# Kernel tuning notes

Measured on AMD Instinct MI355X. Metric: run time of the kernel, lower is better.

## Reference

```python
import jax, jax.numpy as jnp
import numpy as np

DIM = 1024
NUM_HEADS = 16
DPH = DIM // NUM_HEADS
B, S = 4, 2048
LN_EPS = 1e-5


def layer_norm(x, g, b):
    mu = jnp.mean(x, axis=-1, keepdims=True)
    var = jnp.mean((x - mu) ** 2, axis=-1, keepdims=True)
    return (x - mu) * jax.lax.rsqrt(var + LN_EPS) * g + b


def setup_inputs() -> dict:
    key = jax.random.key(0)
    ks = jax.random.split(key, 10)
    sd = 0.02
    return {
        "x": jax.random.normal(ks[0], (B, S, DIM), dtype=jnp.float32),
        "Wq": jax.random.normal(ks[1], (DIM, DIM), dtype=jnp.float32) * sd,
        "Wk": jax.random.normal(ks[2], (DIM, DIM), dtype=jnp.float32) * sd,
        "Wv": jax.random.normal(ks[3], (DIM, DIM), dtype=jnp.float32) * sd,
        "bq": jnp.zeros((DIM,), dtype=jnp.float32),
        "bk": jnp.zeros((DIM,), dtype=jnp.float32),
        "bv": jnp.zeros((DIM,), dtype=jnp.float32),
        "ln1_g": jnp.ones((DIM,), dtype=jnp.float32),
        "ln1_b": jnp.zeros((DIM,), dtype=jnp.float32),
        "W1": jax.random.normal(ks[4], (DIM, 4 * DIM), dtype=jnp.float32) * sd,
        "b1": jnp.zeros((4 * DIM,), dtype=jnp.float32),
        "W2": jax.random.normal(ks[5], (4 * DIM, DIM), dtype=jnp.float32) * sd,
        "b2": jnp.zeros((DIM,), dtype=jnp.float32),
        "ln2_g": jnp.ones((DIM,), dtype=jnp.float32),
        "ln2_b": jnp.zeros((DIM,), dtype=jnp.float32),
    }


def reference(x, Wq, Wk, Wv, bq, bk, bv, ln1_g, ln1_b, W1, b1, W2, b2, ln2_g, ln2_b):
    b, s, d = x.shape
    # QKV projections (heads are independent linears -> one fused GEMM each)
    q = (x @ Wq + bq).reshape(b, s, NUM_HEADS, DPH)
    k = (x @ Wk + bk).reshape(b, s, NUM_HEADS, DPH)
    v = (x @ Wv + bv).reshape(b, s, NUM_HEADS, DPH)
    # Faithful quirk: module scales by 1/sqrt(dph) twice => 1/dph total
    scores = jnp.einsum("bqhd,bkhd->bhqk", q, k) / DPH
    causal = jnp.tril(jnp.ones((s, s), dtype=bool))
    scores = jnp.where(causal, scores, -1e9)
    attn = jax.nn.softmax(scores, axis=-1)
    out_attn = jnp.einsum("bhqk,bkhd->bqhd", attn, v).reshape(b, s, d)
    # Add & Norm 1 (no output projection in original)
    h = layer_norm(out_attn + x, ln1_g, ln1_b)
    # Feed-forward (dropout is identity at eval)
    ffn = jax.nn.relu(h @ W1 + b1) @ W2 + b2
    # Add & Norm 2
    return layer_norm(ffn + h, ln2_g, ln2_b)
```

## Files before the change

### kernel.cpp

```cpp
#include <hip/hip_runtime.h>
#include <hip/hip_bf16.h>

typedef __bf16 bf16_t;
typedef __bf16 bf16x8 __attribute__((ext_vector_type(8)));
typedef __bf16 bf16x4 __attribute__((ext_vector_type(4)));
typedef float  floatx4 __attribute__((ext_vector_type(4)));

#define DIM    1024
#define S_LEN  2048
#define NHEAD  16

template <typename T>
__device__ __forceinline__ bf16x8 load8bf(const T* src) {
  if constexpr (sizeof(T) == 2) {
    return *reinterpret_cast<const bf16x8*>(src);
  } else {
    floatx4 f0 = *reinterpret_cast<const floatx4*>(src);
    floatx4 f1 = *reinterpret_cast<const floatx4*>(src + 4);
    bf16x8 h;
    h[0] = (bf16_t)f0[0]; h[1] = (bf16_t)f0[1];
    h[2] = (bf16_t)f0[2]; h[3] = (bf16_t)f0[3];
    h[4] = (bf16_t)f1[0]; h[5] = (bf16_t)f1[1];
    h[6] = (bf16_t)f1[2]; h[7] = (bf16_t)f1[3];
    return h;
  }
}

__global__ __launch_bounds__(256) void convT3(
    const float* __restrict__ in0, int ldi0, bf16_t* __restrict__ out0,
    const float* __restrict__ in1, int ldi1, bf16_t* __restrict__ out1,
    const float* __restrict__ in2, int ldi2, bf16_t* __restrict__ out2,
    int ldo) {
  __shared__ bf16_t tile[32][33];
  const int z = blockIdx.z;
  const float* in = (z == 0) ? in0 : ((z == 1) ? in1 : in2);
  bf16_t* out = (z == 0) ? out0 : ((z == 1) ? out1 : out2);
  int ldi = (z == 0) ? ldi0 : ((z == 1) ? ldi1 : ldi2);
  int tx = threadIdx.x, ty = threadIdx.y;
  int n0 = blockIdx.x * 32, k0 = blockIdx.y * 32;
#pragma unroll
  for (int i = 0; i < 4; ++i)
    tile[ty + 8 * i][tx] = (bf16_t)in[(size_t)(k0 + ty + 8 * i) * ldi + n0 + tx];
  __syncthreads();
#pragma unroll
  for (int i = 0; i < 4; ++i)
    out[(size_t)(n0 + ty + 8 * i) * ldo + k0 + tx] = tile[tx][ty + 8 * i];
}

#define BM 128
#define BN 128
#define BK 32
#define LSTR 40

template <typename TA>
__global__ __launch_bounds__(256) void gemm_abt(
    const TA* __restrict__ A, int lda,
    const bf16_t* __restrict__ Bt, int zBRow,
    bf16_t* __restrict__ C, int ldc, int zCOff,
    const float* __restrict__ bias0, const float* __restrict__ bias1,
    const float* __restrict__ bias2,
    int K, int relu, int accum) {
  __shared__ bf16_t As[BM * LSTR];
  __shared__ bf16_t Bs[BN * LSTR];
  const int z = blockIdx.z;
  const float* bias = (z == 0) ? bias0 : ((z == 1) ? bias1 : bias2);
  const bf16_t* Bz = Bt + (size_t)z * zBRow * K;
  C += (size_t)z * zCOff;

  const int tid  = threadIdx.x;
  const int lane = tid & 63;
  const int wave = tid >> 6;
  const int wr   = wave >> 1;
  const int wc   = wave & 1;
  const int quad = lane >> 4;
  const int l15  = lane & 15;
  const int m0   = blockIdx.y * BM;
  const int n0   = blockIdx.x * BN;

  floatx4 acc[4][4];
#pragma unroll
  for (int i = 0; i < 4; ++i)
#pragma unroll
    for (int j = 0; j < 4; ++j) acc[i][j] = (floatx4)(0.0f);

  const int kIters = K / BK;
  for (int kt = 0; kt < kIters; ++kt) {
#pragma unroll
    for (int p = 0; p < 2; ++p) {
      int id  = p * 256 + tid;
      int row = id >> 2;
      int c8  = (id & 3) * 8;
      *reinterpret_cast<bf16x8*>(&As[row * LSTR + c8]) =
          load8bf(A + (size_t)(m0 + row) * lda + kt * BK + c8);
      *reinterpret_cast<bf16x8*>(&Bs[row * LSTR + c8]) =
          *reinterpret_cast<const bf16x8*>(Bz + (size_t)(n0 + row) * K + kt * BK + c8);
    }
    __syncthreads();

    bf16x8 a[4], b[4];
#pragma unroll
    for (int i = 0; i < 4; ++i)
      a[i] = *reinterpret_cast<const bf16x8*>(&As[(wr * 64 + i * 16 + l15) * LSTR + quad * 8]);
#pragma unroll
    for (int j = 0; j < 4; ++j)
      b[j] = *reinterpret_cast<const bf16x8*>(&Bs[(wc * 64 + j * 16 + l15) * LSTR + quad * 8]);
#pragma unroll
    for (int i = 0; i < 4; ++i)
#pragma unroll
      for (int j = 0; j < 4; ++j)
        acc[i][j] = __builtin_amdgcn_mfma_f32_16x16x32_bf16(a[i], b[j], acc[i][j], 0, 0, 0);
    __syncthreads();
  }

#pragma unroll
  for (int j = 0; j < 4; ++j) {
    int gn = n0 + wc * 64 + j * 16 + l15;
    float bv = bias ? bias[gn] : 0.0f;
#pragma unroll
    for (int i = 0; i < 4; ++i) {
      int gm = m0 + wr * 64 + i * 16 + quad * 4;
#pragma unroll
      for (int r = 0; r < 4; ++r) {
        float v = acc[i][j][r] + bv;
        if (relu) v = fmaxf(v, 0.0f);
        size_t idx = (size_t)(gm + r) * ldc + gn;
        if (accum) v += (float)C[idx];
        C[idx] = (bf16_t)v;
      }
    }
  }
}

__global__ __launch_bounds__(256) void transpose_v(const bf16_t* __restrict__ in,
                                                   bf16_t* __restrict__ outp) {
  __shared__ bf16_t tile[32][33];
  int tx = threadIdx.x, ty = threadIdx.y;
  int s0 = blockIdx.x * 32, d0 = blockIdx.y * 32, bh = blockIdx.z;
  int z = bh >> 4, h = bh & 15;
  const bf16_t* src = in + (size_t)z * S_LEN * 3072 + 2048 + h * 64;
#pragma unroll
  for (int i = 0; i < 4; ++i)
    tile[ty + 8 * i][tx] = src[(size_t)(s0 + ty + 8 * i) * 3072 + d0 + tx];
  __syncthreads();
  bf16_t* dst = outp + (size_t)bh * 64 * S_LEN;
#pragma unroll
  for (int i = 0; i < 4; ++i)
    dst[(size_t)(d0 + ty + 8 * i) * S_LEN + s0 + tx] = tile[tx][ty + 8 * i];
}

#define TQ  64
#define TK  64
#define AST 72
#define QSCALE 0.02254211f

struct KVregs { bf16x8 k[2]; bf16x8 v[2]; };

__global__ __launch_bounds__(256, 2) void attn_mfma2(
    const bf16_t* __restrict__ qkv, const bf16_t* __restrict__ vt,
    float* __restrict__ out) {
  __shared__ bf16_t QsPs[TQ * AST];
  __shared__ bf16_t Ks[TK * AST];
  __shared__ bf16_t Vs[TK * AST];

  const int tid  = threadIdx.x;
  const int lane = tid & 63;
  const int w    = tid >> 6;
  const int quad = lane >> 4;
  const int l15  = lane & 15;
  const int pi   = blockIdx.x;
  const int h    = blockIdx.y;
  const int z    = blockIdx.z;
  const int qb2[2] = {pi, 31 - pi};
  const bf16_t* qkv_b = qkv + (size_t)z * S_LEN * 3072;
  const bf16_t* vt_bh = vt + ((size_t)z * NHEAD + h) * 64 * S_LEN;
  float* out_b = out + (size_t)z * S_LEN * DIM;

  const int ktEnd = qb2[1] + 1;

  auto kv_load = [&](KVregs& r, int kt) {
#pragma unroll
    for (int p = 0; p < 2; ++p) {
      int id  = p * 256 + tid;
      int row = id >> 3;
      int c8  = (id & 7) * 8;
      r.k[p] = *reinterpret_cast<const bf16x8*>(
          qkv_b + (size_t)(kt * TK + row) * 3072 + 1024 + h * 64 + c8);
      r.v[p] = *reinterpret_cast<const bf16x8*>(
          vt_bh + (size_t)row * S_LEN + kt * TK + c8);
    }
  };
  auto kv_write = [&](KVregs& r) {
#pragma unroll
    for (int p = 0; p < 2; ++p) {
      int id  = p * 256 + tid;
      int row = id >> 3;
      int c8  = (id & 7) * 8;
      *reinterpret_cast<bf16x8*>(&Ks[row * AST + c8]) = r.k[p];
      *reinterpret_cast<bf16x8*>(&Vs[row * AST + c8]) = r.v[p];
    }
  };

  KVregs RA, RB;
  kv_load(RA, 0);

  bf16x8 aq[2][2];
  for (int tile = 0; tile < 2; ++tile) {
    if (tile) __syncthreads();
    const int qg0 = qb2[tile] * TQ;
#pragma unroll
    for (int p = 0; p < 2; ++p) {
      int id  = p * 256 + tid;
      int row = id >> 3;
      int c8  = (id & 7) * 8;
      bf16x8 v = *reinterpret_cast<const bf16x8*>(
          qkv_b + (size_t)(qg0 + row) * 3072 + h * 64 + c8);
      bf16x8 o;
#pragma unroll
      for (int e = 0; e < 8; ++e) o[e] = (bf16_t)((float)v[e] * QSCALE);
      *reinterpret_cast<bf16x8*>(&QsPs[row * AST + c8]) = o;
    }
    __syncthreads();
#pragma unroll
    for (int ks = 0; ks < 2; ++ks)
      aq[tile][ks] = *reinterpret_cast<const bf16x8*>(
          &QsPs[(w * 16 + l15) * AST + ks * 32 + quad * 8]);
  }

  float lp[2][4];
  floatx4 O[2][4];
#pragma unroll
  for (int t = 0; t < 2; ++t)
#pragma unroll
    for (int r = 0; r < 4; ++r) lp[t][r] = 0.0f;
#pragma unroll
  for (int t = 0; t < 2; ++t)
#pragma unroll
    for (int dt = 0; dt < 4; ++dt) O[t][dt] = (floatx4)(0.0f);

  auto step = [&](int kt, KVregs& cur, KVregs& nxt) {
    if (kt + 1 < ktEnd) kv_load(nxt, kt + 1);
    asm volatile("s_waitcnt lgkmcnt(0)" ::: "memory");
    __builtin_amdgcn_s_barrier();
    kv_write(cur);
    asm volatile("s_waitcnt lgkmcnt(0)" ::: "memory");
    __builtin_amdgcn_s_barrier();

    bf16x8 bk[4][2], bv[4][2];
#pragma unroll
    for (int i = 0; i < 4; ++i)
#pragma unroll
      for (int ks = 0; ks < 2; ++ks) {
        bk[i][ks] = *reinterpret_cast<const bf16x8*>(
            &Ks[(i * 16 + l15) * AST + ks * 32 + quad * 8]);
        bv[i][ks] = *reinterpret_cast<const bf16x8*>(
            &Vs[(i * 16 + l15) * AST + ks * 32 + quad * 8]);
      }

#pragma unroll
    for (int tile = 0; tile < 2; ++tile) {
      const int qtb = qb2[tile] * TQ + w * 16;
      if (kt * TK > qtb + 15) continue;

      floatx4 s[4];
      __builtin_amdgcn_s_setprio(1);
#pragma unroll
      for (int ktl = 0; ktl < 4; ++ktl) {
        s[ktl] = __builtin_amdgcn_mfma_f32_16x16x32_bf16(
            aq[tile][0], bk[ktl][0], (floatx4)(0.0f), 0, 0, 0);
        s[ktl] = __builtin_amdgcn_mfma_f32_16x16x32_bf16(
            aq[tile][1], bk[ktl][1], s[ktl], 0, 0, 0);
      }
      __builtin_amdgcn_s_setprio(0);
      if (kt * TK + TK - 1 > qtb) {
#pragma unroll
        for (int ktl = 0; ktl < 4; ++ktl) {
          int gk = kt * TK + ktl * 16 + l15;
#pragma unroll
          for (int r = 0; r < 4; ++r) {
            int gq = qtb + quad * 4 + r;
            if (gk > gq) s[ktl][r] = -1e30f;
          }
        }
      }
#pragma unroll
      for (int ktl = 0; ktl < 4; ++ktl)
#pragma unroll
        for (int r = 0; r < 4; ++r) {
          float p = exp2f(s[ktl][r]);
          lp[tile][r] += p;
          QsPs[(w * 16 + quad * 4 + r) * AST + ktl * 16 + l15] = (bf16_t)p;
        }

      bf16x8 ap0 = *reinterpret_cast<const bf16x8*>(
          &QsPs[(w * 16 + l15) * AST + quad * 8]);
      bf16x8 ap1 = *reinterpret_cast<const bf16x8*>(
          &QsPs[(w * 16 + l15) * AST + 32 + quad * 8]);
      __builtin_amdgcn_s_setprio(1);
#pragma unroll
      for (int dt = 0; dt < 4; ++dt) {
        O[tile][dt] = __builtin_amdgcn_mfma_f32_16x16x32_bf16(
            ap0, bv[dt][0], O[tile][dt], 0, 0, 0);
        O[tile][dt] = __builtin_amdgcn_mfma_f32_16x16x32_bf16(
            ap1, bv[dt][1], O[tile][dt], 0, 0, 0);
      }
      __builtin_amdgcn_s_setprio(0);
    }
  };

  for (int kt = 0; kt < ktEnd; kt += 2) {
    step(kt, RA, RB);
    if (kt + 1 < ktEnd) step(kt + 1, RB, RA);
  }

#pragma unroll
  for (int tile = 0; tile < 2; ++tile) {
    const int qg0 = qb2[tile] * TQ;
    float inv[4];
#pragma unroll
    for (int r = 0; r < 4; ++r) {
      float lv = lp[tile][r];
#pragma unroll
      for (int off = 1; off < 16; off <<= 1) lv += __shfl_xor(lv, off);
      inv[r] = 1.0f / lv;
    }
#pragma unroll
    for (int dt = 0; dt < 4; ++dt)
#pragma unroll
      for (int r = 0; r < 4; ++r)
        out_b[(size_t)(qg0 + w * 16 + quad * 4 + r) * DIM +
              h * 64 + dt * 16 + l15] = O[tile][dt][r] * inv[r];
  }
}

template <typename TA>
__global__ __launch_bounds__(256) void add_ln_k(const TA* a,
                                                const float* b,
                                                const float* __restrict__ g,
                                                const float* __restrict__ be,
                                                float* out) {
  const int row = blockIdx.x;
  const int t   = threadIdx.x;
  const size_t base = (size_t)row * DIM;

  float x[4];
  {
    floatx4 bv = *reinterpret_cast<const floatx4*>(b + base + t * 4);
    if constexpr (sizeof(TA) == 2) {
      bf16x4 av = *reinterpret_cast<const bf16x4*>(a + base + t * 4);
#pragma unroll
      for (int i = 0; i < 4; ++i) x[i] = (float)av[i] + bv[i];
    } else {
      floatx4 av = *reinterpret_cast<const floatx4*>(a + base + t * 4);
#pragma unroll
      for (int i = 0; i < 4; ++i) x[i] = av[i] + bv[i];
    }
  }
  float s1 = 0.0f, s2 = 0.0f;
#pragma unroll
  for (int i = 0; i < 4; ++i) { s1 += x[i]; s2 += x[i] * x[i]; }
#pragma unroll
  for (int off = 32; off; off >>= 1) {
    s1 += __shfl_xor(s1, off);
    s2 += __shfl_xor(s2, off);
  }
  __shared__ float ls1[4], ls2[4];
  if ((t & 63) == 0) { ls1[t >> 6] = s1; ls2[t >> 6] = s2; }
  __syncthreads();
  float S1 = ls1[0] + ls1[1] + ls1[2] + ls1[3];
  float S2 = ls2[0] + ls2[1] + ls2[2] + ls2[3];
  float mu  = S1 * (1.0f / DIM);
  float var = S2 * (1.0f / DIM) - mu * mu;
  float rs  = rsqrtf(var + 1e-5f);
#pragma unroll
  for (int i = 0; i < 4; ++i) {
    int c = t * 4 + i;
    out[base + c] = (x[i] - mu) * rs * g[c] + be[c];
  }
}

extern "C" void kernel_launch(void* const* d_in, const int* in_sizes, int n_in,
                              void* d_out, int out_size, void* d_ws, size_t ws_size,
                              hipStream_t stream) {
  const float* x   = (const float*)d_in[0];
  const float* Wq  = (const float*)d_in[1];
  const float* Wk  = (const float*)d_in[2];
  const float* Wv  = (const float*)d_in[3];
  const float* bq  = (const float*)d_in[4];
  const float* bk  = (const float*)d_in[5];
  const float* bv  = (const float*)d_in[6];
  const float* g1  = (const float*)d_in[7];
  const float* be1 = (const float*)d_in[8];
  const float* W1  = (const float*)d_in[9];
  const float* b1  = (const float*)d_in[10];
  const float* W2  = (const float*)d_in[11];
  const float* b2  = (const float*)d_in[12];
  const float* g2  = (const float*)d_in[13];
  const float* be2 = (const float*)d_in[14];
  float* out = (float*)d_out;
  char*  ws  = (char*)d_ws;

  bf16_t* WqkvT = (bf16_t*)(ws);
  bf16_t* qkv2  = (bf16_t*)(ws + 6291456);
  bf16_t* vt    = (bf16_t*)(ws + 31457280);
  bf16_t* W1Tq  = (bf16_t*)(ws);
  bf16_t* W2Tq  = (bf16_t*)(ws + 2097152);
  bf16_t* mid   = (bf16_t*)(ws + 4194304);
  bf16_t* ffnO  = (bf16_t*)(ws + 20971520);

  dim3 tb(32, 8);
  convT3<<<dim3(32, 32, 3), tb, 0, stream>>>(
      Wq, 1024, WqkvT, Wk, 1024, WqkvT + 1048576, Wv, 1024, WqkvT + 2097152, 1024);

  for (int p = 0; p < 2; ++p) {
    const float* xp   = x   + (size_t)p * 2 * S_LEN * DIM;
    float*       outp = out + (size_t)p * 2 * S_LEN * DIM;
    gemm_abt<float><<<dim3(8, 32, 3), 256, 0, stream>>>(
        xp, 1024, WqkvT, 1024, qkv2, 3072, 1024, bq, bk, bv, 1024, 0, 0);
    transpose_v<<<dim3(64, 2, 32), tb, 0, stream>>>(qkv2, vt);
    attn_mfma2<<<dim3(16, 16, 2), 256, 0, stream>>>(qkv2, vt, outp);
  }
  add_ln_k<float><<<8192, 256, 0, stream>>>(out, x, g1, be1, out);

  for (int q = 0; q < 4; ++q) {
    convT3<<<dim3(32, 32, 2), tb, 0, stream>>>(
        W1 + q * 1024, 4096, W1Tq,
        W2 + (size_t)q * 1024 * 1024, 1024, W2Tq,
        nullptr, 0, nullptr, 1024);
    gemm_abt<float><<<dim3(8, 64, 1), 256, 0, stream>>>(
        out, 1024, W1Tq, 0, mid, 1024, 0, b1 + q * 1024, nullptr, nullptr,
        1024, 1, 0);
    gemm_abt<bf16_t><<<dim3(8, 64, 1), 256, 0, stream>>>(
        mid, 1024, W2Tq, 0, ffnO, 1024, 0, (q == 0) ? b2 : nullptr, nullptr,
        nullptr, 1024, 0, (q > 0) ? 1 : 0);
  }
  add_ln_k<bf16_t><<<8192, 256, 0, stream>>>(ffnO, out, g2, be2, out);
}
```

Measured before the change: 729.1 us.

## Load GEMM tiles with global_load_lds and pre-convert x to bf16

Tile loads for B, and for A when it is bf16, now go straight from global memory into LDS through the global_load_lds builtin, with an unpadded stride. A new conversion kernel turns x into bf16 before the QKV GEMM so that GEMM can use the direct LDS path too. This avoids staging loads through registers and converting fp32 inside the GEMM three times, at the cost of an extra kernel launch and a bf16 buffer. The unpadded LDS layout may cause bank conflicts when the fragments are read. The xbf buffer shares its workspace offset with vt, which looks safe because the conversion runs before transpose_v in each pass.

```diff
diff --git a/kernel.cpp b/kernel.cpp
--- a/kernel.cpp
+++ b/kernel.cpp
@@ -26,6 +26,18 @@
   }
 }
 
+__device__ __forceinline__ void gll16(const bf16_t* g, bf16_t* l) {
+  __builtin_amdgcn_global_load_lds(
+      (const __attribute__((address_space(1))) void*)g,
+      (__attribute__((address_space(3))) void*)l, 16, 0, 0);
+}
+
+__global__ __launch_bounds__(256) void conv_bf(const float* __restrict__ in,
+                                               bf16_t* __restrict__ out) {
+  size_t i = ((size_t)blockIdx.x * 256 + threadIdx.x) * 8;
+  *reinterpret_cast<bf16x8*>(out + i) = load8bf(in + i);
+}
+
 __global__ __launch_bounds__(256) void convT3(
     const float* __restrict__ in0, int ldi0, bf16_t* __restrict__ out0,
     const float* __restrict__ in1, int ldi1, bf16_t* __restrict__ out1,
@@ -60,8 +72,9 @@
     const float* __restrict__ bias0, const float* __restrict__ bias1,
     const float* __restrict__ bias2,
     int K, int relu, int accum) {
+  constexpr int ASTR = (sizeof(TA) == 2) ? BK : LSTR;
   __shared__ bf16_t As[BM * LSTR];
-  __shared__ bf16_t Bs[BN * LSTR];
+  __shared__ bf16_t Bs[BN * BK];
   const int z = blockIdx.z;
   const float* bias = (z == 0) ? bias0 : ((z == 1) ? bias1 : bias2);
   const bf16_t* Bz = Bt + (size_t)z * zBRow * K;
@@ -86,24 +99,37 @@
   const int kIters = K / BK;
   for (int kt = 0; kt < kIters; ++kt) {
 #pragma unroll
-    for (int p = 0; p < 2; ++p) {
-      int id  = p * 256 + tid;
-      int row = id >> 2;
-      int c8  = (id & 3) * 8;
-      *reinterpret_cast<bf16x8*>(&As[row * LSTR + c8]) =
-          load8bf(A + (size_t)(m0 + row) * lda + kt * BK + c8);
-      *reinterpret_cast<bf16x8*>(&Bs[row * LSTR + c8]) =
-          *reinterpret_cast<const bf16x8*>(Bz + (size_t)(n0 + row) * K + kt * BK + c8);
+    for (int i = 0; i < 2; ++i)
+      gll16(Bz + (size_t)(n0 + wave * 32 + i * 16 + (lane >> 2)) * K +
+                kt * BK + (lane & 3) * 8,
+            &Bs[(wave * 32 + i * 16) * BK]);
+    if constexpr (sizeof(TA) == 2) {
+#pragma unroll
+      for (int i = 0; i < 2; ++i)
+        gll16(A + (size_t)(m0 + wave * 32 + i * 16 + (lane >> 2)) * lda +
+                  kt * BK + (lane & 3) * 8,
+              &As[(wave * 32 + i * 16) * BK]);
+    } else {
+#pragma unroll
+      for (int p = 0; p < 2; ++p) {
+        int id  = p * 256 + tid;
+        int row = id >> 2;
+        int c8  = (id & 3) * 8;
+        *reinterpret_cast<bf16x8*>(&As[row * LSTR + c8]) =
+            load8bf(A + (size_t)(m0 + row) * lda + kt * BK + c8);
+      }
     }
     __syncthreads();
 
     bf16x8 a[4], b[4];
 #pragma unroll
     for (int i = 0; i < 4; ++i)
-      a[i] = *reinterpret_cast<const bf16x8*>(&As[(wr * 64 + i * 16 + l15) * LSTR + quad * 8]);
+      a[i] = *reinterpret_cast<const bf16x8*>(
+          &As[(wr * 64 + i * 16 + l15) * ASTR + quad * 8]);
 #pragma unroll
     for (int j = 0; j < 4; ++j)
-      b[j] = *reinterpret_cast<const bf16x8*>(&Bs[(wc * 64 + j * 16 + l15) * LSTR + quad * 8]);
+      b[j] = *reinterpret_cast<const bf16x8*>(
+          &Bs[(wc * 64 + j * 16 + l15) * BK + quad * 8]);
 #pragma unroll
     for (int i = 0; i < 4; ++i)
 #pragma unroll
@@ -402,6 +428,7 @@
   bf16_t* WqkvT = (bf16_t*)(ws);
   bf16_t* qkv2  = (bf16_t*)(ws + 6291456);
   bf16_t* vt    = (bf16_t*)(ws + 31457280);
+  bf16_t* xbf   = (bf16_t*)(ws + 31457280);
   bf16_t* W1Tq  = (bf16_t*)(ws);
   bf16_t* W2Tq  = (bf16_t*)(ws + 2097152);
   bf16_t* mid   = (bf16_t*)(ws + 4194304);
@@ -414,8 +441,9 @@
   for (int p = 0; p < 2; ++p) {
     const float* xp   = x   + (size_t)p * 2 * S_LEN * DIM;
     float*       outp = out + (size_t)p * 2 * S_LEN * DIM;
-    gemm_abt<float><<<dim3(8, 32, 3), 256, 0, stream>>>(
-        xp, 1024, WqkvT, 1024, qkv2, 3072, 1024, bq, bk, bv, 1024, 0, 0);
+    conv_bf<<<2048, 256, 0, stream>>>(xp, xbf);
+    gemm_abt<bf16_t><<<dim3(8, 32, 3), 256, 0, stream>>>(
+        xbf, 1024, WqkvT, 1024, qkv2, 3072, 1024, bq, bk, bv, 1024, 0, 0);
     transpose_v<<<dim3(64, 2, 32), tb, 0, stream>>>(qkv2, vt);
     attn_mfma2<<<dim3(16, 16, 2), 256, 0, stream>>>(qkv2, vt, outp);
   }
```

New measurement: 718.3 us. Within noise of the previous version (-1.5%).
